# Kernel optimization log

Measured on AMD Instinct MI355X. Metric: run time of the kernel, lower is better.

The kernel has to match this reference:

```python
import jax, jax.numpy as jnp
import numpy as np

N_NODES = 50000
N_EDGES = 800000
INPUT_DIM = 8
HIDDEN_DIM = 128


def setup_inputs() -> dict:
    key = jax.random.key(0)
    k = jax.random.split(key, 8)
    x = jax.random.normal(k[0], (N_NODES, INPUT_DIM), dtype=jnp.float32)
    edge_index = jax.random.randint(k[1], (2, N_EDGES), 0, N_NODES, dtype=jnp.int64)
    edge_attr = jax.random.uniform(k[2], (N_EDGES, 1), dtype=jnp.float32)
    node_embedding = jax.random.normal(k[3], (N_NODES, HIDDEN_DIM), dtype=jnp.float32)
    # Linear weights stored as [in, out] so y = x @ W (bias=False everywhere)
    s1 = 1.0 / np.sqrt(INPUT_DIM)
    sh = 1.0 / np.sqrt(HIDDEN_DIM)
    W1 = jax.random.uniform(k[4], (INPUT_DIM, HIDDEN_DIM), jnp.float32, -s1, s1)
    W2 = jax.random.uniform(k[5], (HIDDEN_DIM, HIDDEN_DIM), jnp.float32, -sh, sh)
    W3 = jax.random.uniform(k[6], (HIDDEN_DIM, HIDDEN_DIM), jnp.float32, -sh, sh)
    W4 = jax.random.uniform(k[7], (1, HIDDEN_DIM), jnp.float32, -1.0, 1.0)
    return {"x": x, "edge_index": edge_index, "edge_attr": edge_attr,
            "node_embedding": node_embedding, "W1": W1, "W2": W2, "W3": W3, "W4": W4}


def reference(x, edge_index, edge_attr, node_embedding, W1, W2, W3, W4):
    n = x.shape[0]
    row, col = edge_index[0], edge_index[1]
    # theta_1(x): [N, hidden]
    node_feature_embedding = x @ W1
    # gather neighbor embeddings along edges, scatter-sum to destination rows
    node_embedding_aggr = jax.ops.segment_sum(node_embedding[col], row, num_segments=n)
    # relu(theta_4(edge_attr)): [E, hidden], then scatter-sum to rows
    edge_feature_embedding = jax.nn.relu(edge_attr @ W4)
    edge_embedding_aggr = jax.ops.segment_sum(edge_feature_embedding, row, num_segments=n)
    return jax.nn.relu(node_feature_embedding + node_embedding_aggr @ W2 + edge_embedding_aggr @ W3)
```

## Files before the change

kernel.cpp:

```cpp
#include <hip/hip_runtime.h>

#define N_NODES 50000
#define N_EDGES 800000
#define IN_DIM  8
#define HD      128
#define NREP 16
#define NRANGE 16
#define RANGE_N (N_NODES / NRANGE)
#define N_HISTB (NREP * NRANGE)
#define N_HIST_BLOCKS (N_EDGES / 256)
#define NTILES ((N_NODES + 63) / 64)
#define N_SCAN_BLOCKS ((N_NODES + 255) / 256)
#define GRID_P1 (N_HISTB + NTILES + 1)

typedef unsigned short ushort_t;
typedef unsigned int uint_t;
typedef __attribute__((ext_vector_type(8))) short short8;
typedef __attribute__((ext_vector_type(4))) float float4v;
typedef __attribute__((ext_vector_type(4))) int int4v;
typedef __attribute__((ext_vector_type(2))) uint_t uint2v;

static __device__ inline unsigned short f2bf(float f) {
    unsigned u = __float_as_uint(f);
    unsigned r = (u + 0x7FFF + ((u >> 16) & 1)) >> 16;
    return (unsigned short)r;
}
static __device__ inline float bf2f(unsigned short b) {
    return __uint_as_float(((unsigned)b) << 16);
}

__global__ __launch_bounds__(256, 2)
void phase1_kernel(const float* __restrict__ emb,
                   const float* __restrict__ W2,
                   ushort_t* __restrict__ T16,
                   const int* __restrict__ ei,
                   int* __restrict__ cnt,
                   ushort_t* __restrict__ rank16,
                   const float* __restrict__ W4,
                   const float* __restrict__ W3,
                   float* __restrict__ v3,
                   int* __restrict__ bsums) {
    __shared__ uint_t hcnt[RANGE_N];
    int t = threadIdx.x;

    if (blockIdx.x < N_HISTB) {
        int rep   = blockIdx.x & (NREP - 1);
        int range = blockIdx.x / NREP;
        int rbase = range * RANGE_N;
        for (int i = t; i < RANGE_N; i += 256) hcnt[i] = 0u;
        __syncthreads();
        int g = t >> 6, lane = t & 63;
        int NC = (N_HIST_BLOCKS - rep + NREP - 1) / NREP;
        int j = g;
        int4v rv = {0, 0, 0, 0};
        if (j < NC)
            rv = *(const int4v*)(ei + (rep + j * NREP) * 256 + lane * 4);
        while (j < NC) {
            int jn = j + 4;
            int4v nx = {0, 0, 0, 0};
            if (jn < NC)
                nx = *(const int4v*)(ei + (rep + jn * NREP) * 256 + lane * 4);
            int e0 = (rep + j * NREP) * 256 + lane * 4;
#pragma unroll
            for (int q = 0; q < 4; ++q) {
                int lr = rv[q] - rbase;
                if ((unsigned)lr < (unsigned)RANGE_N) {
                    uint_t rk = atomicAdd(&hcnt[lr], 1u);
                    rank16[e0 + q] = (ushort_t)rk;
                }
            }
            rv = nx; j = jn;
        }
        __syncthreads();
        int* crow = cnt + rep * N_NODES + rbase;
        for (int i = t; i < RANGE_N; i += 256) crow[i] = (int)hcnt[i];
        return;
    }

    if (blockIdx.x == N_HISTB + NTILES) {
        bsums[t] = 0;
        if (t < HD) {
            float acc = 0.f;
            for (int k = 0; k < HD; ++k) {
                float w = W4[k];
                w = w > 0.f ? w : 0.f;
                acc += w * W3[k * HD + t];
            }
            v3[t] = acc;
        }
        return;
    }

    int tt   = blockIdx.x - N_HISTB;
    int wave = t >> 6;
    int lane = t & 63;
    int n16  = lane & 15;
    int quad = lane >> 4;

    int rowbase = tt * 64 + wave * 16;
    int row  = rowbase + n16;
    int rowc = row < N_NODES ? row : N_NODES - 1;
    const float4v* arow = (const float4v*)(emb + (size_t)rowc * HD);

    short8 efrag[4];
#pragma unroll
    for (int ki = 0; ki < 4; ++ki) {
        float4v lo = __builtin_nontemporal_load(&arow[ki * 8 + quad * 2]);
        float4v hi = __builtin_nontemporal_load(&arow[ki * 8 + quad * 2 + 1]);
        short8 a;
        a[0] = (short)f2bf(lo[0]); a[1] = (short)f2bf(lo[1]);
        a[2] = (short)f2bf(lo[2]); a[3] = (short)f2bf(lo[3]);
        a[4] = (short)f2bf(hi[0]); a[5] = (short)f2bf(hi[1]);
        a[6] = (short)f2bf(hi[2]); a[7] = (short)f2bf(hi[3]);
        efrag[ki] = a;
    }

    float4v acc[8];
#pragma unroll
    for (int ct = 0; ct < 8; ++ct) acc[ct] = (float4v){0.f, 0.f, 0.f, 0.f};

    const float* wbase = W2 + (quad * 8) * HD + n16;
#pragma unroll
    for (int ki = 0; ki < 4; ++ki) {
        const float* wk = wbase + ki * 32 * HD;
        short8 wf[8];
#pragma unroll
        for (int ct = 0; ct < 8; ++ct)
#pragma unroll
            for (int j = 0; j < 8; ++j)
                wf[ct][j] = (short)f2bf(wk[j * HD + ct * 16]);
#pragma unroll
        for (int ct = 0; ct < 8; ++ct)
            acc[ct] = __builtin_amdgcn_mfma_f32_16x16x32_bf16(
                wf[ct], efrag[ki], acc[ct], 0, 0, 0);
    }

    if (row < N_NODES) {
        ushort_t* dstu = T16 + (size_t)row * HD + quad * 4;
#pragma unroll
        for (int ct = 0; ct < 8; ++ct) {
            uint2v v;
            v[0] = (uint_t)f2bf(acc[ct][0]) | ((uint_t)f2bf(acc[ct][1]) << 16);
            v[1] = (uint_t)f2bf(acc[ct][2]) | ((uint_t)f2bf(acc[ct][3]) << 16);
            *(uint2v*)(dstu + ct * 16) = v;
        }
    }
}

__global__ void scan1_kernel(const int* __restrict__ cnt,
                             int* __restrict__ off,
                             int* __restrict__ bases,
                             int* __restrict__ bsums) {
    __shared__ int lds[256];
    int t = threadIdx.x;
    int n = blockIdx.x * 256 + t;
    int c[NREP];
    int tsum = 0;
#pragma unroll
    for (int r = 0; r < NREP; ++r) {
        c[r] = (n < N_NODES) ? cnt[r * N_NODES + n] : 0;
        tsum += c[r];
    }
    lds[t] = tsum;
    __syncthreads();
    for (int o = 1; o < 256; o <<= 1) {
        int add = (t >= o) ? lds[t - o] : 0;
        __syncthreads();
        lds[t] += add;
        __syncthreads();
    }
    int ex = lds[t] - tsum;
    int total = lds[255];
    if (n < N_NODES) {
        off[n] = ex;
        int run = ex;
#pragma unroll
        for (int r = 0; r < NREP; ++r) {
            bases[r * N_NODES + n] = run;
            run += c[r];
        }
    }
    for (int bb = blockIdx.x + 1 + t; bb < N_SCAN_BLOCKS; bb += 256)
        atomicAdd(&bsums[bb], total);
}

__global__ void fill_kernel(const int* __restrict__ ei,
                            const float* __restrict__ attr,
                            const ushort_t* __restrict__ rank16,
                            const int* __restrict__ bases,
                            const int* __restrict__ bsums,
                            uint_t* __restrict__ packed) {
    int e = blockIdx.x * 256 + threadIdx.x;
    int rep = (e >> 8) & (NREP - 1);
    int r = ei[e];
    int pos = bases[rep * N_NODES + r] + bsums[r >> 8] + (int)rank16[e];
    uint_t p = ((uint_t)f2bf(attr[e]) << 16) | (uint_t)ei[N_EDGES + e];
    packed[pos] = p;
}

__global__ void aggregate_kernel(const int* __restrict__ off,
                                 const int* __restrict__ bsums,
                                 const uint_t* __restrict__ packed,
                                 const ushort_t* __restrict__ T16,
                                 const float* __restrict__ x,
                                 const float* __restrict__ W1,
                                 const float* __restrict__ v3,
                                 float* __restrict__ out) {
    int tid  = blockIdx.x * 256 + threadIdx.x;
    int node = tid >> 4;
    int lane = tid & 15;
    int s  = off[node] + bsums[node >> 8];
    int e1 = (node + 1 == N_NODES) ? N_EDGES
                                   : off[node + 1] + bsums[(node + 1) >> 8];
    int deg = e1 - s;

    float acc[8];
#pragma unroll
    for (int i = 0; i < 8; ++i) acc[i] = 0.f;
    float ssum = 0.f;

    for (int base = 0; base < deg; base += 16) {
        int rem = deg - base; if (rem > 16) rem = 16;
        uint_t p = 0;
        if (lane < rem) p = __builtin_nontemporal_load(&packed[s + base + lane]);
        ssum += __uint_as_float(p & 0xFFFF0000u);
        int col = (int)(p & 0xFFFFu);
        int j = 0;
        for (; j + 4 <= rem; j += 4) {
            int c0 = __shfl(col, j + 0, 16);
            int c1 = __shfl(col, j + 1, 16);
            int c2 = __shfl(col, j + 2, 16);
            int c3 = __shfl(col, j + 3, 16);
            short8 t0 = ((const short8*)(T16 + (size_t)c0 * HD))[lane];
            short8 t1 = ((const short8*)(T16 + (size_t)c1 * HD))[lane];
            short8 t2 = ((const short8*)(T16 + (size_t)c2 * HD))[lane];
            short8 t3 = ((const short8*)(T16 + (size_t)c3 * HD))[lane];
#pragma unroll
            for (int i = 0; i < 8; ++i)
                acc[i] += (bf2f((ushort_t)t0[i]) + bf2f((ushort_t)t1[i]))
                        + (bf2f((ushort_t)t2[i]) + bf2f((ushort_t)t3[i]));
        }
        for (; j < rem; ++j) {
            int c = __shfl(col, j, 16);
            short8 tv = ((const short8*)(T16 + (size_t)c * HD))[lane];
#pragma unroll
            for (int i = 0; i < 8; ++i)
                acc[i] += bf2f((ushort_t)tv[i]);
        }
    }
    for (int o = 8; o; o >>= 1) ssum += __shfl_xor(ssum, o, 16);

    const float4v* v3p = (const float4v*)v3;
    float4v b0 = v3p[lane * 2], b1 = v3p[lane * 2 + 1];
    acc[0] += ssum * b0[0]; acc[1] += ssum * b0[1];
    acc[2] += ssum * b0[2]; acc[3] += ssum * b0[3];
    acc[4] += ssum * b1[0]; acc[5] += ssum * b1[1];
    acc[6] += ssum * b1[2]; acc[7] += ssum * b1[3];
#pragma unroll
    for (int i = 0; i < IN_DIM; ++i) {
        float xi = x[node * IN_DIM + i];
        const float4v* wp = (const float4v*)(W1 + i * HD);
        float4v w0 = wp[lane * 2], w1 = wp[lane * 2 + 1];
        acc[0] += xi * w0[0]; acc[1] += xi * w0[1];
        acc[2] += xi * w0[2]; acc[3] += xi * w0[3];
        acc[4] += xi * w1[0]; acc[5] += xi * w1[1];
        acc[6] += xi * w1[2]; acc[7] += xi * w1[3];
    }
    float4v o0, o1;
    o0[0] = fmaxf(acc[0], 0.f); o0[1] = fmaxf(acc[1], 0.f);
    o0[2] = fmaxf(acc[2], 0.f); o0[3] = fmaxf(acc[3], 0.f);
    o1[0] = fmaxf(acc[4], 0.f); o1[1] = fmaxf(acc[5], 0.f);
    o1[2] = fmaxf(acc[6], 0.f); o1[3] = fmaxf(acc[7], 0.f);
    float4v* op = (float4v*)(out + (size_t)node * HD);
    __builtin_nontemporal_store(o0, op + lane * 2);
    __builtin_nontemporal_store(o1, op + lane * 2 + 1);
}

extern "C" void kernel_launch(void* const* d_in, const int* in_sizes, int n_in,
                              void* d_out, int out_size, void* d_ws, size_t ws_size,
                              hipStream_t stream) {
    const float* x    = (const float*)d_in[0];
    const int*   ei   = (const int*)  d_in[1];
    const float* attr = (const float*)d_in[2];
    const float* emb  = (const float*)d_in[3];
    const float* W1   = (const float*)d_in[4];
    const float* W2   = (const float*)d_in[5];
    const float* W3   = (const float*)d_in[6];
    const float* W4   = (const float*)d_in[7];
    float* out = (float*)d_out;

    char* w = (char*)d_ws;
    uint_t*   packed = (uint_t*)w;
    ushort_t* T16    = (ushort_t*)(w + (size_t)N_EDGES * 4);
    int*      off    = (int*)((char*)T16 + (size_t)N_NODES * HD * 2);
    int*      bases  = off + N_NODES + 4;
    int*      cnt    = bases + NREP * N_NODES;
    int*      bsums  = cnt + NREP * N_NODES;
    float*    v3     = (float*)(bsums + 256);
    ushort_t* rank16 = (ushort_t*)(v3 + HD);

    phase1_kernel<<<GRID_P1, 256, 0, stream>>>(
        emb, W2, T16, ei, cnt, rank16, W4, W3, v3, bsums);
    scan1_kernel <<<N_SCAN_BLOCKS, 256, 0, stream>>>(cnt, off, bases, bsums);
    fill_kernel  <<<N_HIST_BLOCKS, 256, 0, stream>>>(ei, attr, rank16, bases, bsums, packed);
    aggregate_kernel<<<(N_NODES * 16) / 256, 256, 0, stream>>>(
        off, bsums, packed, T16, x, W1, v3, out);
}
```

Before: 174.7 us.

## Stage W2 bf16 fragments in LDS, deepen gather unroll, nontemporal fill loads

In the GEMM tiles of phase1, the block converts W2 to bf16 MFMA fragments once, cooperatively, into shared memory. Each wave then reads those fragments instead of doing strided global loads and conversions itself. The aggregate kernel's gather loop is unrolled from 4 to 8 neighbor rows per iteration to expose more outstanding loads, and it gets launch bounds of 2 blocks per CU. The fill kernel's streaming reads use nontemporal loads. The extra register pressure from the deeper unroll and the larger shared allocation (32KB) may reduce occupancy.

```diff
diff --git a/kernel.cpp b/kernel.cpp
--- a/kernel.cpp
+++ b/kernel.cpp
@@ -40,10 +40,11 @@
                    const float* __restrict__ W3,
                    float* __restrict__ v3,
                    int* __restrict__ bsums) {
-    __shared__ uint_t hcnt[RANGE_N];
+    __shared__ __align__(16) char shmem[32768];
     int t = threadIdx.x;
 
     if (blockIdx.x < N_HISTB) {
+        uint_t* hcnt = (uint_t*)shmem;
         int rep   = blockIdx.x & (NREP - 1);
         int range = blockIdx.x / NREP;
         int rbase = range * RANGE_N;
@@ -91,11 +92,28 @@
         return;
     }
 
+    short8* sblob = (short8*)shmem;
     int tt   = blockIdx.x - N_HISTB;
     int wave = t >> 6;
     int lane = t & 63;
     int n16  = lane & 15;
     int quad = lane >> 4;
+
+#pragma unroll
+    for (int i = 0; i < 8; ++i) {
+        int slot = t * 8 + i;
+        int f    = slot >> 6;
+        int ln   = slot & 63;
+        int ct = f >> 2, ki = f & 3;
+        int nn = ln & 15, qq = ln >> 4;
+        short8 fr;
+#pragma unroll
+        for (int jj = 0; jj < 8; ++jj) {
+            int k = ki * 32 + qq * 8 + jj;
+            fr[jj] = (short)f2bf(W2[k * HD + ct * 16 + nn]);
+        }
+        sblob[slot] = fr;
+    }
 
     int rowbase = tt * 64 + wave * 16;
     int row  = rowbase + n16;
@@ -119,16 +137,13 @@
 #pragma unroll
     for (int ct = 0; ct < 8; ++ct) acc[ct] = (float4v){0.f, 0.f, 0.f, 0.f};
 
-    const float* wbase = W2 + (quad * 8) * HD + n16;
+    __syncthreads();
 #pragma unroll
     for (int ki = 0; ki < 4; ++ki) {
-        const float* wk = wbase + ki * 32 * HD;
         short8 wf[8];
 #pragma unroll
         for (int ct = 0; ct < 8; ++ct)
-#pragma unroll
-            for (int j = 0; j < 8; ++j)
-                wf[ct][j] = (short)f2bf(wk[j * HD + ct * 16]);
+            wf[ct] = sblob[(ct * 4 + ki) * 64 + lane];
 #pragma unroll
         for (int ct = 0; ct < 8; ++ct)
             acc[ct] = __builtin_amdgcn_mfma_f32_16x16x32_bf16(
@@ -192,20 +207,23 @@
                             uint_t* __restrict__ packed) {
     int e = blockIdx.x * 256 + threadIdx.x;
     int rep = (e >> 8) & (NREP - 1);
-    int r = ei[e];
-    int pos = bases[rep * N_NODES + r] + bsums[r >> 8] + (int)rank16[e];
-    uint_t p = ((uint_t)f2bf(attr[e]) << 16) | (uint_t)ei[N_EDGES + e];
+    int r = __builtin_nontemporal_load(&ei[e]);
+    int pos = bases[rep * N_NODES + r] + bsums[r >> 8]
+            + (int)__builtin_nontemporal_load(&rank16[e]);
+    uint_t p = ((uint_t)f2bf(__builtin_nontemporal_load(&attr[e])) << 16)
+             | (uint_t)__builtin_nontemporal_load(&ei[N_EDGES + e]);
     packed[pos] = p;
 }
 
-__global__ void aggregate_kernel(const int* __restrict__ off,
-                                 const int* __restrict__ bsums,
-                                 const uint_t* __restrict__ packed,
-                                 const ushort_t* __restrict__ T16,
-                                 const float* __restrict__ x,
-                                 const float* __restrict__ W1,
-                                 const float* __restrict__ v3,
-                                 float* __restrict__ out) {
+__global__ __launch_bounds__(256, 2)
+void aggregate_kernel(const int* __restrict__ off,
+                      const int* __restrict__ bsums,
+                      const uint_t* __restrict__ packed,
+                      const ushort_t* __restrict__ T16,
+                      const float* __restrict__ x,
+                      const float* __restrict__ W1,
+                      const float* __restrict__ v3,
+                      float* __restrict__ out) {
     int tid  = blockIdx.x * 256 + threadIdx.x;
     int node = tid >> 4;
     int lane = tid & 15;
@@ -226,19 +244,19 @@
         ssum += __uint_as_float(p & 0xFFFF0000u);
         int col = (int)(p & 0xFFFFu);
         int j = 0;
-        for (; j + 4 <= rem; j += 4) {
-            int c0 = __shfl(col, j + 0, 16);
-            int c1 = __shfl(col, j + 1, 16);
-            int c2 = __shfl(col, j + 2, 16);
-            int c3 = __shfl(col, j + 3, 16);
-            short8 t0 = ((const short8*)(T16 + (size_t)c0 * HD))[lane];
-            short8 t1 = ((const short8*)(T16 + (size_t)c1 * HD))[lane];
-            short8 t2 = ((const short8*)(T16 + (size_t)c2 * HD))[lane];
-            short8 t3 = ((const short8*)(T16 + (size_t)c3 * HD))[lane];
-#pragma unroll
-            for (int i = 0; i < 8; ++i)
-                acc[i] += (bf2f((ushort_t)t0[i]) + bf2f((ushort_t)t1[i]))
-                        + (bf2f((ushort_t)t2[i]) + bf2f((ushort_t)t3[i]));
+        for (; j + 8 <= rem; j += 8) {
+            int cc[8];
+#pragma unroll
+            for (int u = 0; u < 8; ++u) cc[u] = __shfl(col, j + u, 16);
+            short8 tv[8];
+#pragma unroll
+            for (int u = 0; u < 8; ++u)
+                tv[u] = ((const short8*)(T16 + (size_t)cc[u] * HD))[lane];
+#pragma unroll
+            for (int u = 0; u < 8; ++u)
+#pragma unroll
+                for (int i = 0; i < 8; ++i)
+                    acc[i] += bf2f((ushort_t)tv[u][i]);
         }
         for (; j < rem; ++j) {
             int c = __shfl(col, j, 16);
```

After: 190.5 us. 9.0% more time.
